# Optimization experiments

Measured on AMD Instinct MI355X. Metric: run time of the kernel, lower is better.

The kernel has to match this reference:

```python
import jax, jax.numpy as jnp
import numpy as np

B, S, D = 4, 2048, 1024


def setup_inputs() -> dict:
    key = jax.random.key(0)
    kx, kq, kk, kv, km = jax.random.split(key, 5)
    x = jax.random.normal(kx, (B, S, D), dtype=jnp.float32)
    # bias-free Linear weights, torch convention W: (out, in), y = x @ W.T
    Wq = jax.random.normal(kq, (D, D), dtype=jnp.float32) * 0.02
    Wk = jax.random.normal(kk, (D, D), dtype=jnp.float32) * 0.02
    Wv = jax.random.normal(kv, (D, D), dtype=jnp.float32) * 0.02
    # quantum mask: probability vector per batch over seq positions
    q_mask = jax.nn.softmax(jax.random.normal(km, (B, S), dtype=jnp.float32), axis=-1)
    return {"x": x, "Wq": Wq, "Wk": Wk, "Wv": Wv, "q_mask": q_mask}


def reference(x, Wq, Wk, Wv, q_mask):
    # projections (torch Linear: x @ W.T)
    q = jnp.einsum("bsd,ed->bse", x, Wq)
    k = jnp.einsum("bsd,ed->bse", x, Wk)
    v = jnp.einsum("bsd,ed->bse", x, Wv)
    scale = 1.0 / jnp.sqrt(jnp.asarray(D, dtype=x.dtype))
    scores = jnp.einsum("bqe,bke->bqk", q, k) * scale  # (B, S, S)
    # per-row multiplicative quantum mask (mask broadcast over key dim)
    scores = scores * q_mask[:, :, None]
    attn = jax.nn.softmax(scores, axis=-1)
    out = jnp.einsum("bqk,bkd->bqd", attn, v)
    return out
```

## Files before the change

### kernel.cpp

```cpp
#include <hip/hip_runtime.h>
#include <hip/hip_bf16.h>

#define BB 4
#define SS 2048
#define DD 1024

using f32x4  = __attribute__((ext_vector_type(4))) float;
using i32x8  = __attribute__((ext_vector_type(8))) int;

struct f8_t { unsigned char b; };

__device__ __forceinline__ void gld16(const void* g, void* l) {
    __builtin_amdgcn_global_load_lds(
        (const __attribute__((address_space(1))) void*)(g),
        (__attribute__((address_space(3))) void*)(l),
        16, 0, 0);
}

__device__ __forceinline__ void store1(float* p, float v) { *p = v; }
__device__ __forceinline__ void store1(f8_t* p, float v)  {
    p->b = (unsigned char)(__builtin_amdgcn_cvt_pk_fp8_f32(v, v, 0, false) & 0xff);
}

__global__ void cvt_all_kernel(const float* __restrict__ x, const float* __restrict__ Wq,
                               const float* __restrict__ Wk, const float* __restrict__ Wv,
                               unsigned char* __restrict__ x8, unsigned char* __restrict__ w8) {
    const int bid = blockIdx.x;
    const float* src;
    unsigned char* dst;
    long j;
    if (bid < 4096) {
        src = x; dst = x8;
        j = (long)bid * 256 + threadIdx.x;
    } else {
        int lb = bid - 4096;
        int s  = lb >> 9;
        src = (s == 0) ? Wq : (s == 1) ? Wk : Wv;
        dst = w8 + ((size_t)s << 20);
        j = (long)(lb & 511) * 256 + threadIdx.x;
    }
    float4 a = ((const float4*)src)[2 * j];
    float4 b = ((const float4*)src)[2 * j + 1];
    int lo = __builtin_amdgcn_cvt_pk_fp8_f32(a.x, a.y, 0, false);
    lo     = __builtin_amdgcn_cvt_pk_fp8_f32(a.z, a.w, lo, true);
    int hi = __builtin_amdgcn_cvt_pk_fp8_f32(b.x, b.y, 0, false);
    hi     = __builtin_amdgcn_cvt_pk_fp8_f32(b.z, b.w, hi, true);
    ((int2*)dst)[j] = make_int2(lo, hi);
}

__global__ void xsum_kernel(const float* __restrict__ x, float* __restrict__ xsum) {
    int bd = blockIdx.x;
    int b  = bd >> 2, dc = bd & 3;
    int d  = dc * 256 + threadIdx.x;
    int s0 = blockIdx.y * 128;
    const float* p = x + ((size_t)b * SS + s0) * DD + d;
    float acc = 0.f;
    for (int i = 0; i < 128; ++i) acc += p[(size_t)i * DD];
    atomicAdd(&xsum[b * DD + d], acc);
}

__global__ void colsumv_kernel(const float* __restrict__ Wv, const float* __restrict__ xsum,
                               float* __restrict__ colsum) {
    int idx  = blockIdx.x * 4 + (threadIdx.x >> 6);
    int b    = idx >> 10, c = idx & 1023;
    int lane = threadIdx.x & 63;
    const float* wr = Wv + (size_t)c * DD;
    const float* xs = xsum + b * DD;
    float acc = 0.f;
#pragma unroll 4
    for (int d = lane; d < DD; d += 64) acc += wr[d] * xs[d];
#pragma unroll
    for (int off = 32; off; off >>= 1) acc += __shfl_xor(acc, off);
    if (lane == 0) colsum[idx] = acc;
}

template <int MODE, typename CT>
__global__ __launch_bounds__(256, 3) void gemm_f8(
    const unsigned char* __restrict__ A, const unsigned char* __restrict__ B,
    CT* __restrict__ C, int M, int N, int K,
    long batchA, long batchB, long batchC,
    int ldc, int col_shift, long cstride,
    const float* __restrict__ qmask, float* __restrict__ rsum,
    const float* __restrict__ colsum) {
    constexpr int BM = 128, BN = 128, BK = 128;
    constexpr int SCALE_A = (MODE == 3) ? 118 : 127;
    __shared__ __attribute__((aligned(32))) unsigned char As[BM * BK];
    __shared__ __attribute__((aligned(32))) unsigned char Bs[BN * BK];

    const int tid  = threadIdx.x;
    const int lane = tid & 63;
    const int wv   = tid >> 6;
    const int l16  = lane & 15;
    const int quad = lane >> 4;
    const int wm   = wv >> 1;
    const int wn   = wv & 1;

    const int m0 = blockIdx.y * BM;
    const int n0 = blockIdx.x * BN;
    const long z = blockIdx.z;
    const unsigned char* Ab = A + z * batchA;
    const unsigned char* Bb = B + z * batchB;

    const int sw = (quad ^ (l16 & 3)) << 5;

    f32x4 acc[4][4] = {};

    for (int kt = 0; kt < K; kt += BK) {
#pragma unroll
        for (int j = 0; j < 4; ++j) {
            int slot = j * 256 + wv * 64 + lane;
            int r = slot >> 3;
            int c = (slot & 7) ^ ((r & 3) << 1);
            gld16(Ab + (size_t)(m0 + r) * K + (kt + c * 16),
                  As + (size_t)(j * 256 + wv * 64) * 16);
        }
#pragma unroll
        for (int j = 0; j < 4; ++j) {
            int slot = j * 256 + wv * 64 + lane;
            int r = slot >> 3;
            int c = (slot & 7) ^ ((r & 3) << 1);
            gld16(Bb + (size_t)(n0 + r) * K + (kt + c * 16),
                  Bs + (size_t)(j * 256 + wv * 64) * 16);
        }
        asm volatile("s_waitcnt vmcnt(0)" ::: "memory");
        __syncthreads();

        i32x8 af[4], bfr[4];
#pragma unroll
        for (int i = 0; i < 4; ++i)
            af[i] = *(const i32x8*)(As + (wm * 64 + i * 16 + l16) * 128 + sw);
#pragma unroll
        for (int i = 0; i < 4; ++i)
            bfr[i] = *(const i32x8*)(Bs + (wn * 64 + i * 16 + l16) * 128 + sw);

#pragma unroll
        for (int i = 0; i < 4; ++i)
#pragma unroll
            for (int j = 0; j < 4; ++j)
                acc[i][j] = __builtin_amdgcn_mfma_scale_f32_16x16x128_f8f6f4(
                    af[i], bfr[j], acc[i][j], 0, 0, 0, SCALE_A, 0, 127);
        __syncthreads();
    }

    CT* Cb = C + z * batchC;

    if constexpr (MODE == 0) {
#pragma unroll
        for (int mi = 0; mi < 4; ++mi)
#pragma unroll
            for (int ni = 0; ni < 4; ++ni) {
                int colg = n0 + wn * 64 + ni * 16 + l16;
#pragma unroll
                for (int r = 0; r < 4; ++r) {
                    int rowg = m0 + wm * 64 + mi * 16 + quad * 4 + r;
                    store1(Cb + (size_t)rowg * ldc + colg, acc[mi][ni][r]);
                }
            }
    } else if constexpr (MODE == 1) {
#pragma unroll
        for (int mi = 0; mi < 4; ++mi)
#pragma unroll
            for (int ni = 0; ni < 4; ++ni) {
                int colg = n0 + wn * 64 + ni * 16 + l16;
                int cb   = colg >> col_shift;
                int ccol = colg - (cb << col_shift);
#pragma unroll
                for (int r = 0; r < 4; ++r) {
                    int rowg = m0 + wm * 64 + mi * 16 + quad * 4 + r;
                    store1(Cb + (long)cb * cstride + (size_t)rowg * ldc + ccol, acc[mi][ni][r]);
                }
            }
    } else if constexpr (MODE == 2) {
        const float* qm = qmask + (z << 11);
        float* rs = rsum + (z << 11);
#pragma unroll
        for (int mi = 0; mi < 4; ++mi) {
#pragma unroll
            for (int r = 0; r < 4; ++r) {
                int rowg = m0 + wm * 64 + mi * 16 + quad * 4 + r;
                float fac = qm[rowg] * 0.03125f;
                float part = 0.f;
#pragma unroll
                for (int ni = 0; ni < 4; ++ni) {
                    int colg = n0 + wn * 64 + ni * 16 + l16;
                    float t = __expf(acc[mi][ni][r] * fac) - 1.0f;
                    part += t;
                    store1(Cb + (size_t)rowg * ldc + colg, t * 512.0f);
                }
                part += __shfl_xor(part, 1);
                part += __shfl_xor(part, 2);
                part += __shfl_xor(part, 4);
                part += __shfl_xor(part, 8);
                if (l16 == 0) atomicAdd(&rs[rowg], part);
            }
        }
    } else {
        const float* rs = rsum + (z << 11);
        const float* cs = colsum + (z << 10);
#pragma unroll
        for (int mi = 0; mi < 4; ++mi) {
#pragma unroll
            for (int r = 0; r < 4; ++r) {
                int rowg = m0 + wm * 64 + mi * 16 + quad * 4 + r;
                float inv = 1.0f / (2048.0f + rs[rowg]);
#pragma unroll
                for (int ni = 0; ni < 4; ++ni) {
                    int colg = n0 + wn * 64 + ni * 16 + l16;
                    store1(Cb + (size_t)rowg * ldc + colg, (acc[mi][ni][r] + cs[colg]) * inv);
                }
            }
        }
    }
}

extern "C" void kernel_launch(void* const* d_in, const int* in_sizes, int n_in,
                              void* d_out, int out_size, void* d_ws, size_t ws_size,
                              hipStream_t stream) {
    const float* x     = (const float*)d_in[0];
    const float* Wq    = (const float*)d_in[1];
    const float* Wk    = (const float*)d_in[2];
    const float* Wv    = (const float*)d_in[3];
    const float* qmask = (const float*)d_in[4];
    float* out = (float*)d_out;

    const long nx = (long)BB * SS * DD;
    const long nw = (long)DD * DD;

    unsigned char* ws  = (unsigned char*)d_ws;
    unsigned char* x8  = ws;
    unsigned char* w8  = x8 + nx;
    unsigned char* qk8 = w8 + 3 * nw;
    unsigned char* vt8 = qk8 + 2 * nx;
    unsigned char* t8  = vt8 + nx;
    float* xsum   = (float*)(t8 + (long)BB * SS * SS);
    float* rs     = xsum + BB * DD;
    float* colsum = rs + BB * SS;

    hipMemsetAsync(xsum, 0, (size_t)(BB * DD + BB * SS) * sizeof(float), stream);

    cvt_all_kernel<<<dim3(4096 + 1536), dim3(256), 0, stream>>>(x, Wq, Wk, Wv, x8, w8);
    xsum_kernel<<<dim3(16, 16), dim3(256), 0, stream>>>(x, xsum);
    colsumv_kernel<<<dim3(1024), dim3(256), 0, stream>>>(Wv, xsum, colsum);

    gemm_f8<0, f8_t><<<dim3(DD / 128, (BB * SS) / 128, 2), 256, 0, stream>>>(
        x8, w8, (f8_t*)qk8, BB * SS, DD, DD, 0, nw, nx, DD, 31, 0, nullptr, nullptr, nullptr);

    gemm_f8<1, f8_t><<<dim3((BB * SS) / 128, DD / 128, 1), 256, 0, stream>>>(
        w8 + 2 * nw, x8, (f8_t*)vt8, DD, BB * SS, DD, 0, 0, 0, SS, 11, (long)DD * SS,
        nullptr, nullptr, nullptr);

    gemm_f8<2, f8_t><<<dim3(SS / 128, SS / 128, BB), 256, 0, stream>>>(
        qk8, qk8 + nx, (f8_t*)t8, SS, SS, DD, (long)SS * DD, (long)SS * DD, (long)SS * SS,
        SS, 31, 0, qmask, rs, nullptr);

    gemm_f8<3, float><<<dim3(DD / 128, SS / 128, BB), 256, 0, stream>>>(
        t8, vt8, out, SS, DD, SS, (long)SS * SS, (long)DD * SS, (long)SS * DD,
        DD, 31, 0, nullptr, rs, colsum);
}
```

Measured before the change: 214.8 us.

## Double-buffer LDS tiles in fp8 GEMM with two-deep async prefetch

Converts the fp8 MFMA GEMM from a single-buffered load-then-compute loop into a double-buffered pipeline. Tiles for the next two K steps are issued ahead, with partial vmcnt waits and raw barriers. K becomes a compile-time template parameter so the loop fully unrolls. The intent is to hide global-to-LDS latency behind MFMA work; in exchange LDS use doubles to 64KB per block and the occupancy target drops from 3 to 2 blocks.

```diff
diff --git a/kernel.cpp b/kernel.cpp
--- a/kernel.cpp
+++ b/kernel.cpp
@@ -74,18 +74,19 @@
     if (lane == 0) colsum[idx] = acc;
 }
 
-template <int MODE, typename CT>
-__global__ __launch_bounds__(256, 3) void gemm_f8(
+template <int MODE, int KK, typename CT>
+__global__ __launch_bounds__(256, 2) void gemm_f8(
     const unsigned char* __restrict__ A, const unsigned char* __restrict__ B,
-    CT* __restrict__ C, int M, int N, int K,
+    CT* __restrict__ C, int M, int N,
     long batchA, long batchB, long batchC,
     int ldc, int col_shift, long cstride,
     const float* __restrict__ qmask, float* __restrict__ rsum,
     const float* __restrict__ colsum) {
     constexpr int BM = 128, BN = 128, BK = 128;
+    constexpr int NITER = KK / BK;
     constexpr int SCALE_A = (MODE == 3) ? 118 : 127;
-    __shared__ __attribute__((aligned(32))) unsigned char As[BM * BK];
-    __shared__ __attribute__((aligned(32))) unsigned char Bs[BN * BK];
+    __shared__ __attribute__((aligned(32))) unsigned char As[2][BM * BK];
+    __shared__ __attribute__((aligned(32))) unsigned char Bs[2][BN * BK];
 
     const int tid  = threadIdx.x;
     const int lane = tid & 63;
@@ -98,40 +99,56 @@
     const int m0 = blockIdx.y * BM;
     const int n0 = blockIdx.x * BN;
     const long z = blockIdx.z;
-    const unsigned char* Ab = A + z * batchA;
-    const unsigned char* Bb = B + z * batchB;
+    const unsigned char* Ab = A + z * batchA + (size_t)m0 * KK;
+    const unsigned char* Bb = B + z * batchB + (size_t)n0 * KK;
 
     const int sw = (quad ^ (l16 & 3)) << 5;
 
-    f32x4 acc[4][4] = {};
-
-    for (int kt = 0; kt < K; kt += BK) {
+    auto stage = [&](int t, int buf) {
 #pragma unroll
         for (int j = 0; j < 4; ++j) {
             int slot = j * 256 + wv * 64 + lane;
             int r = slot >> 3;
             int c = (slot & 7) ^ ((r & 3) << 1);
-            gld16(Ab + (size_t)(m0 + r) * K + (kt + c * 16),
-                  As + (size_t)(j * 256 + wv * 64) * 16);
+            gld16(Ab + (size_t)r * KK + (t * 128 + c * 16),
+                  &As[buf][(size_t)(j * 256 + wv * 64) * 16]);
         }
 #pragma unroll
         for (int j = 0; j < 4; ++j) {
             int slot = j * 256 + wv * 64 + lane;
             int r = slot >> 3;
             int c = (slot & 7) ^ ((r & 3) << 1);
-            gld16(Bb + (size_t)(n0 + r) * K + (kt + c * 16),
-                  Bs + (size_t)(j * 256 + wv * 64) * 16);
-        }
-        asm volatile("s_waitcnt vmcnt(0)" ::: "memory");
-        __syncthreads();
+            gld16(Bb + (size_t)r * KK + (t * 128 + c * 16),
+                  &Bs[buf][(size_t)(j * 256 + wv * 64) * 16]);
+        }
+    };
+
+    f32x4 acc[4][4] = {};
+
+    stage(0, 0);
+    stage(1, 1);
+
+#pragma unroll
+    for (int kt = 0; kt < NITER; ++kt) {
+        const int cur = kt & 1;
+        if (kt == NITER - 1) {
+            asm volatile("s_waitcnt vmcnt(0)" ::: "memory");
+        } else {
+            asm volatile("s_waitcnt vmcnt(8)" ::: "memory");
+        }
+        asm volatile("s_barrier" ::: "memory");
 
         i32x8 af[4], bfr[4];
 #pragma unroll
         for (int i = 0; i < 4; ++i)
-            af[i] = *(const i32x8*)(As + (wm * 64 + i * 16 + l16) * 128 + sw);
+            af[i] = *(const i32x8*)(&As[cur][(wm * 64 + i * 16 + l16) * 128 + sw]);
 #pragma unroll
         for (int i = 0; i < 4; ++i)
-            bfr[i] = *(const i32x8*)(Bs + (wn * 64 + i * 16 + l16) * 128 + sw);
+            bfr[i] = *(const i32x8*)(&Bs[cur][(wn * 64 + i * 16 + l16) * 128 + sw]);
+
+        asm volatile("s_waitcnt lgkmcnt(0)" ::: "memory");
+        asm volatile("s_barrier" ::: "memory");
+        if (kt + 2 < NITER) stage(kt + 2, cur);
 
 #pragma unroll
         for (int i = 0; i < 4; ++i)
@@ -139,7 +156,6 @@
             for (int j = 0; j < 4; ++j)
                 acc[i][j] = __builtin_amdgcn_mfma_scale_f32_16x16x128_f8f6f4(
                     af[i], bfr[j], acc[i][j], 0, 0, 0, SCALE_A, 0, 127);
-        __syncthreads();
     }
 
     CT* Cb = C + z * batchC;
@@ -242,18 +258,18 @@
     xsum_kernel<<<dim3(16, 16), dim3(256), 0, stream>>>(x, xsum);
     colsumv_kernel<<<dim3(1024), dim3(256), 0, stream>>>(Wv, xsum, colsum);
 
-    gemm_f8<0, f8_t><<<dim3(DD / 128, (BB * SS) / 128, 2), 256, 0, stream>>>(
-        x8, w8, (f8_t*)qk8, BB * SS, DD, DD, 0, nw, nx, DD, 31, 0, nullptr, nullptr, nullptr);
-
-    gemm_f8<1, f8_t><<<dim3((BB * SS) / 128, DD / 128, 1), 256, 0, stream>>>(
-        w8 + 2 * nw, x8, (f8_t*)vt8, DD, BB * SS, DD, 0, 0, 0, SS, 11, (long)DD * SS,
+    gemm_f8<0, DD, f8_t><<<dim3(DD / 128, (BB * SS) / 128, 2), 256, 0, stream>>>(
+        x8, w8, (f8_t*)qk8, BB * SS, DD, 0, nw, nx, DD, 31, 0, nullptr, nullptr, nullptr);
+
+    gemm_f8<1, DD, f8_t><<<dim3((BB * SS) / 128, DD / 128, 1), 256, 0, stream>>>(
+        w8 + 2 * nw, x8, (f8_t*)vt8, DD, BB * SS, 0, 0, 0, SS, 11, (long)DD * SS,
         nullptr, nullptr, nullptr);
 
-    gemm_f8<2, f8_t><<<dim3(SS / 128, SS / 128, BB), 256, 0, stream>>>(
-        qk8, qk8 + nx, (f8_t*)t8, SS, SS, DD, (long)SS * DD, (long)SS * DD, (long)SS * SS,
+    gemm_f8<2, DD, f8_t><<<dim3(SS / 128, SS / 128, BB), 256, 0, stream>>>(
+        qk8, qk8 + nx, (f8_t*)t8, SS, SS, (long)SS * DD, (long)SS * DD, (long)SS * SS,
         SS, 31, 0, qmask, rs, nullptr);
 
-    gemm_f8<3, float><<<dim3(DD / 128, SS / 128, BB), 256, 0, stream>>>(
-        t8, vt8, out, SS, DD, SS, (long)SS * SS, (long)DD * SS, (long)SS * DD,
+    gemm_f8<3, SS, float><<<dim3(DD / 128, SS / 128, BB), 256, 0, stream>>>(
+        t8, vt8, out, SS, DD, (long)SS * SS, (long)DD * SS, (long)SS * DD,
         DD, 31, 0, nullptr, rs, colsum);
 }
```

Result: slower. 293.7 us (+36.7%).

## Load GEMM fragments directly from global memory, drop LDS staging

Applied to the files above, without the earlier changes.

The fp8 GEMM no longer stages tiles through shared memory with global_load_lds and barriers. Each lane now reads its 32-byte MFMA operand fragments straight from global memory, and the K loop is templated on a compile-time length and fully unrolled. This removes LDS traffic, the waitcnt and both __syncthreads per K step, and lets the compiler schedule loads early. In exchange, operands are re-read from global or L2 by each wave instead of being shared across the block, which increases memory traffic and register pressure.

```diff
diff --git a/kernel.cpp b/kernel.cpp
--- a/kernel.cpp
+++ b/kernel.cpp
@@ -9,13 +9,6 @@
 using i32x8  = __attribute__((ext_vector_type(8))) int;
 
 struct f8_t { unsigned char b; };
-
-__device__ __forceinline__ void gld16(const void* g, void* l) {
-    __builtin_amdgcn_global_load_lds(
-        (const __attribute__((address_space(1))) void*)(g),
-        (__attribute__((address_space(3))) void*)(l),
-        16, 0, 0);
-}
 
 __device__ __forceinline__ void store1(float* p, float v) { *p = v; }
 __device__ __forceinline__ void store1(f8_t* p, float v)  {
@@ -74,18 +67,16 @@
     if (lane == 0) colsum[idx] = acc;
 }
 
-template <int MODE, typename CT>
+template <int MODE, int KK, typename CT>
 __global__ __launch_bounds__(256, 3) void gemm_f8(
     const unsigned char* __restrict__ A, const unsigned char* __restrict__ B,
-    CT* __restrict__ C, int M, int N, int K,
+    CT* __restrict__ C,
     long batchA, long batchB, long batchC,
     int ldc, int col_shift, long cstride,
     const float* __restrict__ qmask, float* __restrict__ rsum,
     const float* __restrict__ colsum) {
-    constexpr int BM = 128, BN = 128, BK = 128;
+    constexpr int NITER = KK / 128;
     constexpr int SCALE_A = (MODE == 3) ? 118 : 127;
-    __shared__ __attribute__((aligned(32))) unsigned char As[BM * BK];
-    __shared__ __attribute__((aligned(32))) unsigned char Bs[BN * BK];
 
     const int tid  = threadIdx.x;
     const int lane = tid & 63;
@@ -95,43 +86,24 @@
     const int wm   = wv >> 1;
     const int wn   = wv & 1;
 
-    const int m0 = blockIdx.y * BM;
-    const int n0 = blockIdx.x * BN;
+    const int m0 = blockIdx.y * 128;
+    const int n0 = blockIdx.x * 128;
     const long z = blockIdx.z;
-    const unsigned char* Ab = A + z * batchA;
-    const unsigned char* Bb = B + z * batchB;
-
-    const int sw = (quad ^ (l16 & 3)) << 5;
+
+    const unsigned char* Ap = A + z * batchA + (size_t)(m0 + wm * 64 + l16) * KK + quad * 32;
+    const unsigned char* Bp = B + z * batchB + (size_t)(n0 + wn * 64 + l16) * KK + quad * 32;
 
     f32x4 acc[4][4] = {};
 
-    for (int kt = 0; kt < K; kt += BK) {
-#pragma unroll
-        for (int j = 0; j < 4; ++j) {
-            int slot = j * 256 + wv * 64 + lane;
-            int r = slot >> 3;
-            int c = (slot & 7) ^ ((r & 3) << 1);
-            gld16(Ab + (size_t)(m0 + r) * K + (kt + c * 16),
-                  As + (size_t)(j * 256 + wv * 64) * 16);
-        }
-#pragma unroll
-        for (int j = 0; j < 4; ++j) {
-            int slot = j * 256 + wv * 64 + lane;
-            int r = slot >> 3;
-            int c = (slot & 7) ^ ((r & 3) << 1);
-            gld16(Bb + (size_t)(n0 + r) * K + (kt + c * 16),
-                  Bs + (size_t)(j * 256 + wv * 64) * 16);
-        }
-        asm volatile("s_waitcnt vmcnt(0)" ::: "memory");
-        __syncthreads();
-
+#pragma unroll
+    for (int kt = 0; kt < NITER; ++kt) {
         i32x8 af[4], bfr[4];
 #pragma unroll
         for (int i = 0; i < 4; ++i)
-            af[i] = *(const i32x8*)(As + (wm * 64 + i * 16 + l16) * 128 + sw);
+            af[i] = *(const i32x8*)(Ap + (size_t)i * 16 * KK + kt * 128);
 #pragma unroll
         for (int i = 0; i < 4; ++i)
-            bfr[i] = *(const i32x8*)(Bs + (wn * 64 + i * 16 + l16) * 128 + sw);
+            bfr[i] = *(const i32x8*)(Bp + (size_t)i * 16 * KK + kt * 128);
 
 #pragma unroll
         for (int i = 0; i < 4; ++i)
@@ -139,7 +111,6 @@
             for (int j = 0; j < 4; ++j)
                 acc[i][j] = __builtin_amdgcn_mfma_scale_f32_16x16x128_f8f6f4(
                     af[i], bfr[j], acc[i][j], 0, 0, 0, SCALE_A, 0, 127);
-        __syncthreads();
     }
 
     CT* Cb = C + z * batchC;
@@ -242,18 +213,18 @@
     xsum_kernel<<<dim3(16, 16), dim3(256), 0, stream>>>(x, xsum);
     colsumv_kernel<<<dim3(1024), dim3(256), 0, stream>>>(Wv, xsum, colsum);
 
-    gemm_f8<0, f8_t><<<dim3(DD / 128, (BB * SS) / 128, 2), 256, 0, stream>>>(
-        x8, w8, (f8_t*)qk8, BB * SS, DD, DD, 0, nw, nx, DD, 31, 0, nullptr, nullptr, nullptr);
-
-    gemm_f8<1, f8_t><<<dim3((BB * SS) / 128, DD / 128, 1), 256, 0, stream>>>(
-        w8 + 2 * nw, x8, (f8_t*)vt8, DD, BB * SS, DD, 0, 0, 0, SS, 11, (long)DD * SS,
+    gemm_f8<0, DD, f8_t><<<dim3(DD / 128, (BB * SS) / 128, 2), 256, 0, stream>>>(
+        x8, w8, (f8_t*)qk8, 0, nw, nx, DD, 31, 0, nullptr, nullptr, nullptr);
+
+    gemm_f8<1, DD, f8_t><<<dim3((BB * SS) / 128, DD / 128, 1), 256, 0, stream>>>(
+        w8 + 2 * nw, x8, (f8_t*)vt8, 0, 0, 0, SS, 11, (long)DD * SS,
         nullptr, nullptr, nullptr);
 
-    gemm_f8<2, f8_t><<<dim3(SS / 128, SS / 128, BB), 256, 0, stream>>>(
-        qk8, qk8 + nx, (f8_t*)t8, SS, SS, DD, (long)SS * DD, (long)SS * DD, (long)SS * SS,
+    gemm_f8<2, DD, f8_t><<<dim3(SS / 128, SS / 128, BB), 256, 0, stream>>>(
+        qk8, qk8 + nx, (f8_t*)t8, (long)SS * DD, (long)SS * DD, (long)SS * SS,
         SS, 31, 0, qmask, rs, nullptr);
 
-    gemm_f8<3, float><<<dim3(DD / 128, SS / 128, BB), 256, 0, stream>>>(
-        t8, vt8, out, SS, DD, SS, (long)SS * SS, (long)DD * SS, (long)SS * DD,
+    gemm_f8<3, SS, float><<<dim3(DD / 128, SS / 128, BB), 256, 0, stream>>>(
+        t8, vt8, out, (long)SS * SS, (long)DD * SS, (long)SS * DD,
         DD, 31, 0, nullptr, rs, colsum);
 }
```

Result: slower. 542.0 us (+152.3%).
